# Kernel tuning notes

Measured on AMD Instinct MI355X. Metric: run time of the kernel, lower is better.

The kernel has to match this reference:

```python
import jax, jax.numpy as jnp
import numpy as np
from jax import lax

# sym8 analysis low-pass filter (pywt.Wavelet('sym8').dec_lo, matches MATLAB Lo_D)
FL = 16
DEC_LO = np.array([-0.0033824159510061256, -0.0005421323317911481, 0.03169508781149298,
                   0.007607487324917605, -0.1432942383508097, -0.061273359067658524,
                   0.4813596512583722, 0.7771857517005235, 0.3644418948353314,
                   -0.051945838107709037, -0.027219029917056003, 0.049137179673607506,
                   0.003808752013890615, -0.01495225833704823, -0.0003029205147213668,
                   0.0018899503327594609])
REC_LO = DEC_LO[::-1]
REC_HI = ((-1.0) ** np.arange(FL)) * DEC_LO  # qmf: rec_hi[k] = (-1)^k * rec_lo[FL-1-k]
DEC_HI = REC_HI[::-1]
# lax.conv does correlation, np.convolve flips -> store flipped filters
_DEC_K = jnp.asarray(np.stack([DEC_LO[::-1], DEC_HI[::-1]])[:, None, :], dtype=jnp.float32)  # (2,1,16)
_REC_K = jnp.asarray(np.stack([REC_LO[::-1], REC_HI[::-1]])[None, :, :], dtype=jnp.float32)  # (1,2,16)
DN = ('NCH', 'OIH', 'NCH')


def _dwt(x):
    # single-level pywt dwt, mode='symmetric': pad FL-1 each side, full conv, take odd indices
    B, C, S = x.shape
    xe = jnp.pad(x.reshape(B * C, 1, S), ((0, 0), (0, 0), (FL - 1, FL - 1)), mode='symmetric')[..., 1:]
    y = lax.conv_general_dilated(xe, _DEC_K, (2,), 'VALID', dimension_numbers=DN)
    L = y.shape[-1]  # floor((S + FL - 1)/2)
    y = y.reshape(B, C, 2, L)
    return y[:, :, 0], y[:, :, 1]


def _idwt(a, d):
    # single-level pywt idwt: upsample (len 2L-1), full conv, trim FL-2 each side
    B, C, L = a.shape
    c = jnp.stack([a, d], axis=2).reshape(B * C, 2, L)
    y = lax.conv_general_dilated(c, _REC_K, (1,), [(1, 1)], lhs_dilation=(2,), dimension_numbers=DN)
    return y.reshape(B, C, y.shape[-1])  # length 2L - FL + 2


def _wavedec(x, level):
    ds = []
    a = x
    for _ in range(level):
        a, d = _dwt(a)
        ds.append(d)
    return a, ds[::-1]  # coarsest first, matching pywt [cA_n, cD_n, ..., cD_1]


def _waverec(a, ds):
    for d in ds:
        if a.shape[-1] == d.shape[-1] + 1:  # static shapes -> Python if is jit-safe
            a = a[..., :-1]
        a = _idwt(a, d)
    return a


def _c1(x, w, b):
    # 1x1 conv: w (O,C), x (B,C,L)
    return jnp.einsum('oc,bcl->bol', w, x) + b[:, None]


def _inorm(x, eps=1e-5):
    m = jnp.mean(x, axis=-1, keepdims=True)
    v = jnp.mean((x - m) ** 2, axis=-1, keepdims=True)
    return (x - m) * lax.rsqrt(v + eps)


def _block(x, w_w, w_b, ca_w, ca_b, cd_w, cd_b, m1_w, m1_b, m2_w, m2_b):
    xn = _inorm(x)
    xs = lax.conv_general_dilated(xn, w_w, (1,), [(1, 1)], dimension_numbers=DN) + w_b[:, None]
    level = cd_w.shape[0]
    a, ds = _wavedec(xn, level)
    a = _c1(a, ca_w, ca_b)
    ds = [_c1(d, cd_w[i], cd_b[i]) for i, d in enumerate(ds)]
    xw = _waverec(a, ds)[..., : xs.shape[-1]]
    xo = x + jax.nn.gelu(xw + xs, approximate=False)
    xon = _inorm(xo)
    h = jax.nn.gelu(_c1(xon, m1_w, m1_b), approximate=False)
    return xo + _c1(h, m2_w, m2_b)


def _forward(x, lift_w, lift_b, blk_w_w, blk_w_b, blk_ca_w, blk_ca_b, blk_cd_w, blk_cd_b,
             blk_m1_w, blk_m1_b, blk_m2_w, blk_m2_b, p1_w, p1_b, p2_w, p2_b):
    B, S = x.shape
    grid = jnp.broadcast_to(jnp.linspace(-1.0, 1.0, S, dtype=x.dtype)[None, None, :], (B, 1, S))
    h = jnp.concatenate([x[:, None, :], grid], axis=1)  # (B, 2, S)
    h = _c1(h, lift_w, lift_b)
    for i in range(blk_w_w.shape[0]):
        h = _block(h, blk_w_w[i], blk_w_b[i], blk_ca_w[i], blk_ca_b[i], blk_cd_w[i],
                   blk_cd_b[i], blk_m1_w[i], blk_m1_b[i], blk_m2_w[i], blk_m2_b[i])
    h = jax.nn.gelu(_c1(h, p1_w, p1_b), approximate=False)
    return _c1(h, p2_w, p2_b)


def setup_inputs():
    key = jax.random.key(0)
    ks = jax.random.split(key, 17)
    B, S, C, NB, LV = 16, 8192, 64, 4, 4
    H = 2 * C  # mlp_expansion=2
    f = jnp.float32
    rn = lambda k, shape, s: jax.random.normal(k, shape, dtype=f) * s
    return {
        'x': jax.random.normal(ks[0], (B, S), dtype=f),
        'lift_w': rn(ks[1], (C, 2), 0.5), 'lift_b': rn(ks[2], (C,), 0.05),
        'blk_w_w': rn(ks[3], (NB, C, C, 3), 0.07), 'blk_w_b': rn(ks[4], (NB, C), 0.05),
        'blk_ca_w': rn(ks[5], (NB, C, C), 0.12), 'blk_ca_b': rn(ks[6], (NB, C), 0.05),
        'blk_cd_w': rn(ks[7], (NB, LV, C, C), 0.12), 'blk_cd_b': rn(ks[8], (NB, LV, C), 0.05),
        'blk_m1_w': rn(ks[9], (NB, H, C), 0.12), 'blk_m1_b': rn(ks[10], (NB, H), 0.05),
        'blk_m2_w': rn(ks[11], (NB, C, H), 0.08), 'blk_m2_b': rn(ks[12], (NB, C), 0.05),
        'p1_w': rn(ks[13], (C // 2, C), 0.12), 'p1_b': rn(ks[14], (C // 2,), 0.05),
        'p2_w': rn(ks[15], (C, C // 2), 0.17), 'p2_b': rn(ks[16], (C,), 0.05),
    }


def reference(x, lift_w, lift_b, blk_w_w, blk_w_b, blk_ca_w, blk_ca_b, blk_cd_w, blk_cd_b,
              blk_m1_w, blk_m1_b, blk_m2_w, blk_m2_b, p1_w, p1_b, p2_w, p2_b):
    return _forward(x, lift_w, lift_b, blk_w_w, blk_w_b, blk_ca_w, blk_ca_b, blk_cd_w,
                    blk_cd_b, blk_m1_w, blk_m1_b, blk_m2_w, blk_m2_b, p1_w, p1_b, p2_w, p2_b)
```

## Files before the change

### kernel.cpp

```cpp
#include <hip/hip_runtime.h>
#include <math.h>

#define S_LEN 8192
#define B_N   16
#define NBC   1024
#define L1v 4103
#define L2v 2059
#define L3v 1037
#define L4v 526
#define LB1 4104
#define LB2 2064
#define LB3 1040
#define LB4 528

#define OFF_CONV 0
#define OFF_M1   49152
#define OFF_M2   81920
#define OFF_CD   114688
#define OFF_CA   180224
#define OFF_P1   196608
#define OFF_P2   198656
#define WTOT     200704

typedef __attribute__((ext_vector_type(8))) short bf16x8;
typedef __attribute__((ext_vector_type(4))) float f32x4;

__constant__ float c_dlo[16] = {
    -0.0033824159510061256f, -0.0005421323317911481f,  0.03169508781149298f,
     0.007607487324917605f,  -0.1432942383508097f,    -0.061273359067658524f,
     0.4813596512583722f,     0.7771857517005235f,     0.3644418948353314f,
    -0.05194583810770904f,   -0.027219029917056003f,   0.049137179673607506f,
     0.003808752013890615f,  -0.01495225833704823f,   -0.0003029205147213668f,
     0.0018899503327594609f
};
__constant__ float c_dhi[16] = {
    -0.0018899503327594609f, -0.0003029205147213668f,  0.01495225833704823f,
     0.003808752013890615f,  -0.049137179673607506f,  -0.027219029917056003f,
     0.05194583810770904f,    0.3644418948353314f,    -0.7771857517005235f,
     0.4813596512583722f,     0.061273359067658524f,  -0.1432942383508097f,
    -0.007607487324917605f,   0.03169508781149298f,    0.0005421323317911481f,
    -0.0033824159510061256f
};

__device__ __forceinline__ float gelu1(float x) {
    return 0.5f * x * (1.0f + erff(x * 0.70710678118654752f));
}
__device__ __forceinline__ float4 load4g(const float* __restrict__ row, int l, int L) {
    float4 v;
    if (l >= 0 && l + 3 < L) {
        v = *(const float4*)(row + l);
    } else {
        v.x = (l     >= 0 && l     < L) ? row[l]     : 0.f;
        v.y = (l + 1 >= 0 && l + 1 < L) ? row[l + 1] : 0.f;
        v.z = (l + 2 >= 0 && l + 2 < L) ? row[l + 2] : 0.f;
        v.w = (l + 3 >= 0 && l + 3 < L) ? row[l + 3] : 0.f;
    }
    return v;
}
__device__ __forceinline__ ushort f2bf(float f) {
    uint u = __float_as_uint(f);
    u += 0x7fffu + ((u >> 16) & 1u);
    return (ushort)(u >> 16);
}
__device__ __forceinline__ uint pack2bf(float a, float b) {
    return (uint)f2bf(a) | ((uint)f2bf(b) << 16);
}
__device__ __forceinline__ float bfu(ushort u) {
    return __uint_as_float(((uint)u) << 16);
}

__global__ __launch_bounds__(256) void prep_kernel(const float* __restrict__ convW,
                                                   const float* __restrict__ m1,
                                                   const float* __restrict__ m2,
                                                   const float* __restrict__ cd,
                                                   const float* __restrict__ ca,
                                                   const float* __restrict__ p1,
                                                   const float* __restrict__ p2,
                                                   ushort* __restrict__ wbuf) {
    int idx = blockIdx.x * 256 + threadIdx.x;
    if (idx >= WTOT) return;
    float v;
    if (idx < OFF_M1) {
        int i = idx / 12288, r = idx % 12288;
        int o = r / 192, k = r % 192;
        int tap = k >> 6, c = k & 63;
        v = convW[i * 12288 + o * 192 + c * 3 + tap];
    } else if (idx < OFF_M2) v = m1[idx - OFF_M1];
    else if (idx < OFF_CD)   v = m2[idx - OFF_M2];
    else if (idx < OFF_CA)   v = cd[idx - OFF_CD];
    else if (idx < OFF_P1)   v = ca[idx - OFF_CA];
    else if (idx < OFF_P2)   v = p1[idx - OFF_P1];
    else                     v = p2[idx - OFF_P2];
    wbuf[idx] = f2bf(v);
}

__global__ __launch_bounds__(256) void lift_kernel(const float* __restrict__ x,
                                                   const float* __restrict__ w,
                                                   const float* __restrict__ bias,
                                                   float* __restrict__ out) {
    int idx = blockIdx.x * 256 + threadIdx.x;
    int s = idx & (S_LEN - 1);
    int r = idx >> 13;
    int o = r & 63;
    int b = r >> 6;
    float g = -1.0f + 2.0f * (float)s / (float)(S_LEN - 1);
    out[idx] = fmaf(w[o * 2 + 0], x[b * S_LEN + s], fmaf(w[o * 2 + 1], g, bias[o]));
}

__global__ __launch_bounds__(256) void stats_kernel(const float* __restrict__ in,
                                                    float2* __restrict__ stats) {
    const int base = blockIdx.x * S_LEN;
    const int tid = threadIdx.x;
    float s = 0.f, ss = 0.f;
#pragma unroll
    for (int i = 0; i < 8; ++i) {
        float4 v = *(const float4*)(in + base + (tid + i * 256) * 4);
        s += v.x + v.y + v.z + v.w;
        ss = fmaf(v.x, v.x, fmaf(v.y, v.y, fmaf(v.z, v.z, fmaf(v.w, v.w, ss))));
    }
    for (int off = 32; off > 0; off >>= 1) {
        s  += __shfl_down(s, off, 64);
        ss += __shfl_down(ss, off, 64);
    }
    __shared__ float sh[8];
    int lane = tid & 63, wv = tid >> 6;
    if (lane == 0) { sh[wv] = s; sh[4 + wv] = ss; }
    __syncthreads();
    if (tid == 0) {
        float tot  = sh[0] + sh[1] + sh[2] + sh[3];
        float tot2 = sh[4] + sh[5] + sh[6] + sh[7];
        float mean = tot * (1.0f / S_LEN);
        float var  = tot2 * (1.0f / S_LEN) - mean * mean;
        stats[blockIdx.x] = make_float2(mean, rsqrtf(var + 1e-5f));
    }
}

#define CWP 200
#define CXP 72

__global__ __launch_bounds__(256) void conv3_mfma_kernel(const float* __restrict__ in,
                                                         ushort* __restrict__ out,
                                                         const ushort* __restrict__ Wbf,
                                                         const float* __restrict__ bias,
                                                         const float2* __restrict__ stats) {
    __shared__ ushort sW[64 * CWP];
    __shared__ ushort sXt[144 * CXP];
    const int b = blockIdx.y;
    const int n0 = blockIdx.x * 128;
    const int tid = threadIdx.x;

    {
        const int o = tid >> 2, q = tid & 3;
        const uint4* src = (const uint4*)(Wbf + o * 192 + q * 48);
        uint4* dst = (uint4*)(sW + o * CWP + q * 48);
#pragma unroll
        for (int i = 0; i < 6; ++i) dst[i] = src[i];
    }
    {
        const int ch = tid >> 2, q = tid & 3;
        const int rowi = b * 64 + ch;
        const float2 st = stats[rowi];
        const float* row = in + (size_t)rowi * S_LEN;
#pragma unroll
        for (int i = 0; i < 9; ++i) {
            int p = q * 36 + i * 4;
            int l = n0 - 8 + p;
            float4 v;
            if (l >= 0 && l + 3 < S_LEN) {
                v = *(const float4*)(row + l);
                v.x = (v.x - st.x) * st.y; v.y = (v.y - st.x) * st.y;
                v.z = (v.z - st.x) * st.y; v.w = (v.w - st.x) * st.y;
            } else {
                v.x = (l     >= 0 && l     < S_LEN) ? (row[l]     - st.x) * st.y : 0.f;
                v.y = (l + 1 >= 0 && l + 1 < S_LEN) ? (row[l + 1] - st.x) * st.y : 0.f;
                v.z = (l + 2 >= 0 && l + 2 < S_LEN) ? (row[l + 2] - st.x) * st.y : 0.f;
                v.w = (l + 3 >= 0 && l + 3 < S_LEN) ? (row[l + 3] - st.x) * st.y : 0.f;
            }
            sXt[(p + 0) * CXP + ch] = f2bf(v.x);
            sXt[(p + 1) * CXP + ch] = f2bf(v.y);
            sXt[(p + 2) * CXP + ch] = f2bf(v.z);
            sXt[(p + 3) * CXP + ch] = f2bf(v.w);
        }
    }
    __syncthreads();

    const int w = tid >> 6, l = tid & 63, g = l >> 4, c = l & 15;
    f32x4 acc[2][4];
#pragma unroll
    for (int mt = 0; mt < 4; ++mt) {
        float4 bv = *(const float4*)(bias + 16 * mt + 4 * g);
#pragma unroll
        for (int t = 0; t < 2; ++t) {
            acc[t][mt][0] = bv.x; acc[t][mt][1] = bv.y;
            acc[t][mt][2] = bv.z; acc[t][mt][3] = bv.w;
        }
    }
#pragma unroll
    for (int kk = 0; kk < 6; ++kk) {
        const int tap = kk >> 1;
        bf16x8 af[4];
#pragma unroll
        for (int mt = 0; mt < 4; ++mt)
            af[mt] = *(bf16x8*)(sW + (16 * mt + c) * CWP + kk * 32 + 8 * g);
#pragma unroll
        for (int t = 0; t < 2; ++t) {
            const int nl = 32 * w + 16 * t + c;
            const int p = nl + tap + 7;
            bf16x8 xb = *(bf16x8*)(sXt + p * CXP + (kk & 1) * 32 + 8 * g);
#pragma unroll
            for (int mt = 0; mt < 4; ++mt)
                acc[t][mt] = __builtin_amdgcn_mfma_f32_16x16x32_bf16(af[mt], xb, acc[t][mt], 0, 0, 0);
        }
    }
#pragma unroll
    for (int t = 0; t < 2; ++t) {
        const int nl = 32 * w + 16 * t + c;
#pragma unroll
        for (int mt = 0; mt < 4; ++mt)
#pragma unroll
            for (int r = 0; r < 4; ++r) {
                int m = 16 * mt + 4 * g + r;
                out[((size_t)(b * 64 + m)) * S_LEN + n0 + nl] = f2bf(acc[t][mt][r]);
            }
    }
}

#define WMP 72
#define WXP 136

__global__ __launch_bounds__(256) void wmix_kernel(ushort* __restrict__ d1,
                                                   ushort* __restrict__ d2,
                                                   ushort* __restrict__ d3,
                                                   ushort* __restrict__ d4,
                                                   ushort* __restrict__ a4,
                                                   const ushort* __restrict__ cdbf,
                                                   const float* __restrict__ cd_b,
                                                   const ushort* __restrict__ cabf,
                                                   const float* __restrict__ ca_b) {
    __shared__ ushort sW[64 * WMP];
    __shared__ ushort sX[64 * WXP];
    const int b = blockIdx.y;
    const int t = blockIdx.x;
    ushort* buf; const ushort* W; const float* bias; int L, LP, l0;
    if (t < 33)      { buf = d1; W = cdbf + 3 * 4096; bias = cd_b + 3 * 64; L = L1v; LP = LB1; l0 = t * 128; }
    else if (t < 50) { buf = d2; W = cdbf + 2 * 4096; bias = cd_b + 2 * 64; L = L2v; LP = LB2; l0 = (t - 33) * 128; }
    else if (t < 59) { buf = d3; W = cdbf + 1 * 4096; bias = cd_b + 1 * 64; L = L3v; LP = LB3; l0 = (t - 50) * 128; }
    else if (t < 64) { buf = d4; W = cdbf;            bias = cd_b;          L = L4v; LP = LB4; l0 = (t - 59) * 128; }
    else             { buf = a4; W = cabf;            bias = ca_b;          L = L4v; LP = LB4; l0 = (t - 64) * 128; }
    const int tid = threadIdx.x;
    {
        int row = tid >> 2, q = tid & 3;
        const uint4* src = (const uint4*)(W + row * 64 + q * 16);
        uint4* dst = (uint4*)(sW + row * WMP + q * 16);
        dst[0] = src[0]; dst[1] = src[1];
    }
    {
        int ch = tid >> 2, part = tid & 3;
        const ushort* src = buf + ((size_t)(b * 64 + ch)) * LP;
#pragma unroll
        for (int i = 0; i < 4; ++i) {
            int l = l0 + part * 32 + 8 * i;
            ushort* dst = sX + ch * WXP + part * 32 + 8 * i;
            if (l + 8 <= L) {
                *(uint4*)dst = *(const uint4*)(src + l);
            } else {
#pragma unroll
                for (int j = 0; j < 8; ++j)
                    dst[j] = (l + j < L) ? src[l + j] : (ushort)0;
            }
        }
    }
    __syncthreads();
    const int w = tid >> 6, l = tid & 63, g = l >> 4, c = l & 15;
    f32x4 acc[2][4];
#pragma unroll
    for (int mt = 0; mt < 4; ++mt) {
        float4 bv = *(const float4*)(bias + 16 * mt + 4 * g);
#pragma unroll
        for (int tt = 0; tt < 2; ++tt) {
            acc[tt][mt][0] = bv.x; acc[tt][mt][1] = bv.y;
            acc[tt][mt][2] = bv.z; acc[tt][mt][3] = bv.w;
        }
    }
#pragma unroll
    for (int kk = 0; kk < 2; ++kk) {
        bf16x8 af[4];
#pragma unroll
        for (int mt = 0; mt < 4; ++mt)
            af[mt] = *(bf16x8*)(sW + (16 * mt + c) * WMP + kk * 32 + 8 * g);
#pragma unroll
        for (int tt = 0; tt < 2; ++tt) {
            const int nl = 32 * w + 16 * tt + c;
            bf16x8 xb;
#pragma unroll
            for (int j = 0; j < 8; ++j)
                xb[j] = (short)sX[(kk * 32 + 8 * g + j) * WXP + nl];
#pragma unroll
            for (int mt = 0; mt < 4; ++mt)
                acc[tt][mt] = __builtin_amdgcn_mfma_f32_16x16x32_bf16(af[mt], xb, acc[tt][mt], 0, 0, 0);
        }
    }
#pragma unroll
    for (int tt = 0; tt < 2; ++tt) {
        const int nl = 32 * w + 16 * tt + c;
        if (l0 + nl < L) {
#pragma unroll
            for (int mt = 0; mt < 4; ++mt)
#pragma unroll
                for (int r = 0; r < 4; ++r) {
                    int m = 16 * mt + 4 * g + r;
                    buf[((size_t)(b * 64 + m)) * LP + l0 + nl] = f2bf(acc[tt][mt][r]);
                }
        }
    }
}

#define W1P 72
#define W2P 136
#define XP  66
#define MP  136

__global__ __launch_bounds__(256) void mlp_kernel(float* __restrict__ A,
                                                  const float2* __restrict__ stats,
                                                  const ushort* __restrict__ W1bf,
                                                  const float* __restrict__ b1,
                                                  const ushort* __restrict__ W2bf,
                                                  const float* __restrict__ b2) {
    __shared__ ushort sW1[128 * W1P];
    __shared__ ushort sW2[64 * W2P];
    __shared__ ushort sX [64 * XP];
    __shared__ ushort sMid[64 * MP];
    const int b  = blockIdx.y;
    const int n0 = blockIdx.x * 64;
    const int tid = threadIdx.x;

    {
#pragma unroll
        for (int e = tid; e < 1024; e += 256) {
            int row = e >> 3, q = e & 7;
            *(uint4*)(sW1 + row * W1P + q * 8) = *(const uint4*)(W1bf + row * 64 + q * 8);
        }
    }
    {
#pragma unroll
        for (int e = tid; e < 1024; e += 256) {
            int row = e >> 4, q = e & 15;
            *(uint4*)(sW2 + row * W2P + q * 8) = *(const uint4*)(W2bf + row * 128 + q * 8);
        }
    }
    {
        int ch = tid >> 2, part = tid & 3;
        float2 st = stats[b * 64 + ch];
        const float* src = A + ((size_t)(b * 64 + ch)) * S_LEN + n0 + part * 16;
        uint* dst = (uint*)(sX + ch * XP + part * 16);
#pragma unroll
        for (int i = 0; i < 4; ++i) {
            float4 v = *(const float4*)(src + 4 * i);
            v.x = (v.x - st.x) * st.y; v.y = (v.y - st.x) * st.y;
            v.z = (v.z - st.x) * st.y; v.w = (v.w - st.x) * st.y;
            dst[2 * i]     = pack2bf(v.x, v.y);
            dst[2 * i + 1] = pack2bf(v.z, v.w);
        }
    }
    __syncthreads();

    const int w = tid >> 6;
    const int l = tid & 63;
    const int g = l >> 4;
    const int c = l & 15;
    const int nl = 16 * w + c;

    bf16x8 xb[2];
#pragma unroll
    for (int kk = 0; kk < 2; ++kk)
#pragma unroll
        for (int j = 0; j < 8; ++j)
            xb[kk][j] = (short)sX[(kk * 32 + 8 * g + j) * XP + nl];

    f32x4 acc1[8];
#pragma unroll
    for (int mt = 0; mt < 8; ++mt) {
        float4 bv = *(const float4*)(b1 + 16 * mt + 4 * g);
        acc1[mt][0] = bv.x; acc1[mt][1] = bv.y; acc1[mt][2] = bv.z; acc1[mt][3] = bv.w;
    }
#pragma unroll
    for (int kk = 0; kk < 2; ++kk) {
#pragma unroll
        for (int mt = 0; mt < 8; ++mt) {
            bf16x8 af = *(bf16x8*)(sW1 + (16 * mt + c) * W1P + kk * 32 + 8 * g);
            acc1[mt] = __builtin_amdgcn_mfma_f32_16x16x32_bf16(af, xb[kk], acc1[mt], 0, 0, 0);
        }
    }
#pragma unroll
    for (int mt = 0; mt < 8; ++mt) {
        uint* mp = (uint*)(sMid + nl * MP + 16 * mt + 4 * g);
        mp[0] = pack2bf(gelu1(acc1[mt][0]), gelu1(acc1[mt][1]));
        mp[1] = pack2bf(gelu1(acc1[mt][2]), gelu1(acc1[mt][3]));
    }

    bf16x8 mb[4];
#pragma unroll
    for (int kk = 0; kk < 4; ++kk)
        mb[kk] = *(bf16x8*)(sMid + nl * MP + kk * 32 + 8 * g);

    f32x4 acc2[4];
#pragma unroll
    for (int mt = 0; mt < 4; ++mt) {
        float4 bv = *(const float4*)(b2 + 16 * mt + 4 * g);
        acc2[mt][0] = bv.x; acc2[mt][1] = bv.y; acc2[mt][2] = bv.z; acc2[mt][3] = bv.w;
    }
#pragma unroll
    for (int kk = 0; kk < 4; ++kk) {
#pragma unroll
        for (int mt = 0; mt < 4; ++mt) {
            bf16x8 af = *(bf16x8*)(sW2 + (16 * mt + c) * W2P + kk * 32 + 8 * g);
            acc2[mt] = __builtin_amdgcn_mfma_f32_16x16x32_bf16(af, mb[kk], acc2[mt], 0, 0, 0);
        }
    }
#pragma unroll
    for (int mt = 0; mt < 4; ++mt) {
#pragma unroll
        for (int r = 0; r < 4; ++r) {
            int m = 16 * mt + 4 * g + r;
            float* p = A + ((size_t)(b * 64 + m)) * S_LEN + n0 + nl;
            *p = acc2[mt][r] + *p;
        }
    }
}

#define HXP 66
#define HMP 40

__global__ __launch_bounds__(256) void head_kernel(const float* __restrict__ A,
                                                   float* __restrict__ out,
                                                   const ushort* __restrict__ W1bf,
                                                   const float* __restrict__ b1,
                                                   const ushort* __restrict__ W2bf,
                                                   const float* __restrict__ b2) {
    __shared__ ushort sW1[32 * 72];
    __shared__ ushort sW2[64 * HMP];
    __shared__ ushort sX [64 * HXP];
    __shared__ ushort sMid[64 * HMP];
    const int b = blockIdx.y, n0 = blockIdx.x * 64, tid = threadIdx.x;
    {
        int row = tid >> 3, q = tid & 7;
        *(uint4*)(sW1 + row * 72 + q * 8) = *(const uint4*)(W1bf + row * 64 + q * 8);
    }
    {
        int row = tid >> 2, q = tid & 3;
        *(uint4*)(sW2 + row * HMP + q * 8) = *(const uint4*)(W2bf + row * 32 + q * 8);
    }
    {
        int ch = tid >> 2, part = tid & 3;
        const float* src = A + ((size_t)(b * 64 + ch)) * S_LEN + n0 + part * 16;
        uint* dst = (uint*)(sX + ch * HXP + part * 16);
#pragma unroll
        for (int i = 0; i < 4; ++i) {
            float4 v = *(const float4*)(src + 4 * i);
            dst[2 * i] = pack2bf(v.x, v.y); dst[2 * i + 1] = pack2bf(v.z, v.w);
        }
    }
    __syncthreads();
    const int w = tid >> 6, l = tid & 63, g = l >> 4, c = l & 15;
    const int nl = 16 * w + c;
    bf16x8 xb[2];
#pragma unroll
    for (int kk = 0; kk < 2; ++kk)
#pragma unroll
        for (int j = 0; j < 8; ++j)
            xb[kk][j] = (short)sX[(kk * 32 + 8 * g + j) * HXP + nl];
    f32x4 acc1[2];
#pragma unroll
    for (int mt = 0; mt < 2; ++mt) {
        float4 bv = *(const float4*)(b1 + 16 * mt + 4 * g);
        acc1[mt][0] = bv.x; acc1[mt][1] = bv.y; acc1[mt][2] = bv.z; acc1[mt][3] = bv.w;
    }
#pragma unroll
    for (int kk = 0; kk < 2; ++kk)
#pragma unroll
        for (int mt = 0; mt < 2; ++mt) {
            bf16x8 af = *(bf16x8*)(sW1 + (16 * mt + c) * 72 + kk * 32 + 8 * g);
            acc1[mt] = __builtin_amdgcn_mfma_f32_16x16x32_bf16(af, xb[kk], acc1[mt], 0, 0, 0);
        }
#pragma unroll
    for (int mt = 0; mt < 2; ++mt)
#pragma unroll
        for (int r = 0; r < 4; ++r)
            sMid[nl * HMP + 16 * mt + 4 * g + r] = f2bf(gelu1(acc1[mt][r]));
    bf16x8 mb = *(bf16x8*)(sMid + nl * HMP + 8 * g);
    f32x4 acc2[4];
#pragma unroll
    for (int mt = 0; mt < 4; ++mt) {
        float4 bv = *(const float4*)(b2 + 16 * mt + 4 * g);
        acc2[mt][0] = bv.x; acc2[mt][1] = bv.y; acc2[mt][2] = bv.z; acc2[mt][3] = bv.w;
    }
#pragma unroll
    for (int mt = 0; mt < 4; ++mt) {
        bf16x8 af = *(bf16x8*)(sW2 + (16 * mt + c) * HMP + 8 * g);
        acc2[mt] = __builtin_amdgcn_mfma_f32_16x16x32_bf16(af, mb, acc2[mt], 0, 0, 0);
    }
#pragma unroll
    for (int mt = 0; mt < 4; ++mt)
#pragma unroll
        for (int r = 0; r < 4; ++r) {
            int m = 16 * mt + 4 * g + r;
            out[((size_t)(b * 64 + m)) * S_LEN + n0 + nl] = acc2[mt][r];
        }
}

__device__ __forceinline__ void dwt8_core(const float* __restrict__ xb,
                                          float* __restrict__ lo, float* __restrict__ hi) {
#pragma unroll
    for (int j = 0; j < 8; ++j) {
        float l0 = 0.f, h0 = 0.f;
#pragma unroll
        for (int k = 0; k < 16; ++k) {
            float v = xb[2 * j + k + 2];
            l0 = fmaf(v, c_dlo[15 - k], l0);
            h0 = fmaf(v, c_dhi[15 - k], h0);
        }
        lo[j] = l0; hi[j] = h0;
    }
}

__device__ __forceinline__ void store_bf8(ushort* __restrict__ dst, int t0, int Lout,
                                          const float* __restrict__ v) {
    if (t0 + 8 <= Lout) {
        uint4 u;
        u.x = pack2bf(v[0], v[1]); u.y = pack2bf(v[2], v[3]);
        u.z = pack2bf(v[4], v[5]); u.w = pack2bf(v[6], v[7]);
        *(uint4*)(dst + t0) = u;
    } else {
#pragma unroll
        for (int j = 0; j < 8; ++j)
            if (t0 + j < Lout) dst[t0 + j] = f2bf(v[j]);
    }
}

__device__ __forceinline__ void dwt_lds_v2(const float* __restrict__ in, int Sin,
                                           float* __restrict__ aout,
                                           ushort* __restrict__ dout_g, int Lout, int tid) {
    const int NT = (Lout + 7) >> 3;
    for (int g = tid; g < NT; g += 256) {
        float xb[32];
        const int base = 16 * g - 16;
        if (base >= 0 && base + 32 <= Sin) {
#pragma unroll
            for (int q = 0; q < 8; ++q)
                *(float4*)(xb + 4 * q) = *(const float4*)(in + base + 4 * q);
        } else {
#pragma unroll
            for (int loc = 0; loc < 32; ++loc) {
                int i = base + loc;
                i = (i < 0) ? (-1 - i) : i;
                i = (i >= Sin) ? (2 * Sin - 1 - i) : i;
                xb[loc] = in[i];
            }
        }
        float lo[8], hi[8];
        dwt8_core(xb, lo, hi);
        const int t0 = 8 * g;
        if (t0 + 8 <= Lout) {
            *(float4*)(aout + t0)     = make_float4(lo[0], lo[1], lo[2], lo[3]);
            *(float4*)(aout + t0 + 4) = make_float4(lo[4], lo[5], lo[6], lo[7]);
        } else {
#pragma unroll
            for (int j = 0; j < 8; ++j) if (t0 + j < Lout) aout[t0 + j] = lo[j];
        }
        store_bf8(dout_g, t0, Lout, hi);
    }
}

__global__ __launch_bounds__(256) void dwt_full_kernel(const float* __restrict__ A,
                                                       const float2* __restrict__ stats,
                                                       ushort* __restrict__ d1,
                                                       ushort* __restrict__ d2,
                                                       ushort* __restrict__ d3,
                                                       ushort* __restrict__ d4,
                                                       ushort* __restrict__ a4) {
    __shared__ float bufA[4104];
    __shared__ float bufB[2064];
    const int row = blockIdx.x;
    const int tid = threadIdx.x;
    const float2 st = stats[row];
    const float* x = A + (size_t)row * S_LEN;
    ushort* d1r = d1 + (size_t)row * LB1;

    for (int g = tid; g < 513; g += 256) {
        const int base = 16 * g - 16;
        float xb[32];
        if (base >= 0 && base + 32 <= S_LEN) {
#pragma unroll
            for (int q = 0; q < 8; ++q) {
                float4 v = *(const float4*)(x + base + 4 * q);
                v.x = (v.x - st.x) * st.y; v.y = (v.y - st.x) * st.y;
                v.z = (v.z - st.x) * st.y; v.w = (v.w - st.x) * st.y;
                *(float4*)(xb + 4 * q) = v;
            }
        } else {
#pragma unroll
            for (int loc = 0; loc < 32; ++loc) {
                int i = base + loc;
                i = (i < 0) ? (-1 - i) : i;
                i = (i >= S_LEN) ? (2 * S_LEN - 1 - i) : i;
                xb[loc] = (x[i] - st.x) * st.y;
            }
        }
        float lo[8], hi[8];
        dwt8_core(xb, lo, hi);
        const int t0 = 8 * g;
#pragma unroll
        for (int j = 0; j < 8; ++j)
            if (t0 + j < L1v) bufA[t0 + j] = lo[j];
        store_bf8(d1r, t0, L1v, hi);
    }
    __syncthreads();
    dwt_lds_v2(bufA, L1v, bufB, d2 + (size_t)row * LB2, L2v, tid);
    __syncthreads();
    dwt_lds_v2(bufB, L2v, bufA, d3 + (size_t)row * LB3, L3v, tid);
    __syncthreads();
    dwt_lds_v2(bufA, L3v, bufB, d4 + (size_t)row * LB4, L4v, tid);
    __syncthreads();
    ushort* a4r = a4 + (size_t)row * LB4;
    for (int g = tid; g < 66; g += 256) {
        const int t0 = 8 * g;
        float v[8];
#pragma unroll
        for (int j = 0; j < 8; ++j)
            v[j] = (t0 + j < L4v) ? bufB[t0 + j] : 0.f;
        store_bf8(a4r, t0, 528, v);
    }
}

__device__ __forceinline__ void idwt8_regs(const float* __restrict__ a,
                                           const float* __restrict__ d,
                                           int g, int Lc, float* __restrict__ y) {
    float av[12], dv[12];
    const int m0 = 4 * g;
    if (m0 + 12 <= Lc) {
#pragma unroll
        for (int q = 0; q < 3; ++q) {
            *(float4*)(av + 4 * q) = *(const float4*)(a + m0 + 4 * q);
            *(float4*)(dv + 4 * q) = *(const float4*)(d + m0 + 4 * q);
        }
    } else {
#pragma unroll
        for (int jj = 0; jj < 12; ++jj) {
            int m = m0 + jj;
            bool ok = (m < Lc);
            av[jj] = ok ? a[m] : 0.f;
            dv[jj] = ok ? d[m] : 0.f;
        }
    }
#pragma unroll
    for (int e = 0; e < 4; ++e) {
        float ye = 0.f, yo = 0.f;
#pragma unroll
        for (int j = 0; j < 8; ++j) {
            ye = fmaf(av[e + j], c_dlo[2 * j + 1], ye);
            ye = fmaf(dv[e + j], c_dlo[14 - 2 * j], ye);
            yo = fmaf(av[e + j], c_dlo[2 * j], yo);
            yo = fmaf(dv[e + j], -c_dlo[15 - 2 * j], yo);
        }
        y[2 * e] = ye;
        y[2 * e + 1] = yo;
    }
}

__device__ __forceinline__ void idwt_lds_v2(const float* __restrict__ a,
                                            const float* __restrict__ d,
                                            int Lc, int Lout, float* __restrict__ out, int tid) {
    const int NT = (Lout + 7) >> 3;
    for (int g = tid; g < NT; g += 256) {
        float y[8];
        idwt8_regs(a, d, g, Lc, y);
        const int t0 = 8 * g;
        if (t0 + 8 <= Lout) {
            *(float4*)(out + t0)     = make_float4(y[0], y[1], y[2], y[3]);
            *(float4*)(out + t0 + 4) = make_float4(y[4], y[5], y[6], y[7]);
        } else {
#pragma unroll
            for (int j = 0; j < 8; ++j) if (t0 + j < Lout) out[t0 + j] = y[j];
        }
    }
}

__device__ __forceinline__ void gload_lds_bf(const ushort* __restrict__ src, int Lv,
                                             float* __restrict__ dst, int tid) {
    const int NG = (Lv + 7) >> 3;
    for (int g = tid; g < NG; g += 256) {
        uint4 u = *(const uint4*)(src + 8 * g);
        float v[8];
        v[0] = bfu((ushort)u.x); v[1] = bfu((ushort)(u.x >> 16));
        v[2] = bfu((ushort)u.y); v[3] = bfu((ushort)(u.y >> 16));
        v[4] = bfu((ushort)u.z); v[5] = bfu((ushort)(u.z >> 16));
        v[6] = bfu((ushort)u.w); v[7] = bfu((ushort)(u.w >> 16));
        const int t0 = 8 * g;
#pragma unroll
        for (int j = 0; j < 8; ++j)
            dst[t0 + j] = (t0 + j < Lv) ? v[j] : 0.f;
    }
}

__global__ __launch_bounds__(256) void idwt_full_kernel(const ushort* __restrict__ a4,
                                                        const ushort* __restrict__ d4,
                                                        const ushort* __restrict__ d3,
                                                        const ushort* __restrict__ d2,
                                                        const ushort* __restrict__ d1,
                                                        float* __restrict__ h,
                                                        const ushort* __restrict__ xs,
                                                        float2* __restrict__ statsOut) {
    __shared__ float bufY[4104];
    __shared__ float bufA[4104];
    __shared__ float bufD[4104];
    const int row = blockIdx.x;
    const int tid = threadIdx.x;

    gload_lds_bf(a4 + (size_t)row * LB4, L4v, bufA, tid);
    gload_lds_bf(d4 + (size_t)row * LB4, L4v, bufD, tid);
    __syncthreads();
    idwt_lds_v2(bufA, bufD, L4v, 1038, bufY, tid);
    __syncthreads();
    gload_lds_bf(d3 + (size_t)row * LB3, L3v, bufD, tid);
    __syncthreads();
    idwt_lds_v2(bufY, bufD, L3v, 2060, bufA, tid);
    __syncthreads();
    gload_lds_bf(d2 + (size_t)row * LB2, L2v, bufD, tid);
    __syncthreads();
    idwt_lds_v2(bufA, bufD, L2v, 4104, bufY, tid);
    __syncthreads();
    gload_lds_bf(d1 + (size_t)row * LB1, L1v, bufD, tid);
    __syncthreads();

    float* hrow = h + (size_t)row * S_LEN;
    const ushort* srow = xs + (size_t)row * S_LEN;
    float s = 0.f, ss = 0.f;
#pragma unroll
    for (int it = 0; it < 4; ++it) {
        const int g = it * 256 + tid;
        float y[8];
        idwt8_regs(bufY, bufD, g, L1v, y);
        const int t0 = 8 * g;
#pragma unroll
        for (int q = 0; q < 2; ++q) {
            uint2 sp = *(const uint2*)(srow + t0 + 4 * q);
            float4 hv = *(const float4*)(hrow + t0 + 4 * q);
            hv.x += gelu1(y[4 * q + 0] + bfu((ushort)sp.x));
            hv.y += gelu1(y[4 * q + 1] + bfu((ushort)(sp.x >> 16)));
            hv.z += gelu1(y[4 * q + 2] + bfu((ushort)sp.y));
            hv.w += gelu1(y[4 * q + 3] + bfu((ushort)(sp.y >> 16)));
            *(float4*)(hrow + t0 + 4 * q) = hv;
            s += hv.x + hv.y + hv.z + hv.w;
            ss = fmaf(hv.x, hv.x, fmaf(hv.y, hv.y, fmaf(hv.z, hv.z, fmaf(hv.w, hv.w, ss))));
        }
    }
    for (int off = 32; off > 0; off >>= 1) {
        s  += __shfl_down(s, off, 64);
        ss += __shfl_down(ss, off, 64);
    }
    __syncthreads();
    int lane = tid & 63, wv = tid >> 6;
    if (lane == 0) { bufA[wv] = s; bufA[4 + wv] = ss; }
    __syncthreads();
    if (tid == 0) {
        float tot  = bufA[0] + bufA[1] + bufA[2] + bufA[3];
        float tot2 = bufA[4] + bufA[5] + bufA[6] + bufA[7];
        float mean = tot * (1.0f / S_LEN);
        float var  = tot2 * (1.0f / S_LEN) - mean * mean;
        statsOut[row] = make_float2(mean, rsqrtf(var + 1e-5f));
    }
}

extern "C" void kernel_launch(void* const* d_in, const int* in_sizes, int n_in,
                              void* d_out, int out_size, void* d_ws, size_t ws_size,
                              hipStream_t stream) {
    const float* x       = (const float*)d_in[0];
    const float* lift_w  = (const float*)d_in[1];
    const float* lift_b  = (const float*)d_in[2];
    const float* blk_w_w = (const float*)d_in[3];
    const float* blk_w_b = (const float*)d_in[4];
    const float* blk_ca_w= (const float*)d_in[5];
    const float* blk_ca_b= (const float*)d_in[6];
    const float* blk_cd_w= (const float*)d_in[7];
    const float* blk_cd_b= (const float*)d_in[8];
    const float* blk_m1_w= (const float*)d_in[9];
    const float* blk_m1_b= (const float*)d_in[10];
    const float* blk_m2_w= (const float*)d_in[11];
    const float* blk_m2_b= (const float*)d_in[12];
    const float* p1_w    = (const float*)d_in[13];
    const float* p1_b    = (const float*)d_in[14];
    const float* p2_w    = (const float*)d_in[15];
    const float* p2_b    = (const float*)d_in[16];

    float* ws = (float*)d_ws;
    const size_t T32 = (size_t)NBC * S_LEN;
    float* A  = ws;
    ushort* Cc = (ushort*)(ws + T32);
    ushort* d1 = Cc + T32;
    ushort* d2 = d1 + (size_t)NBC * LB1;
    ushort* d3 = d2 + (size_t)NBC * LB2;
    ushort* d4 = d3 + (size_t)NBC * LB3;
    ushort* a4 = d4 + (size_t)NBC * LB4;
    float2* statsBuf = (float2*)(a4 + (size_t)NBC * LB4 + 8);
    ushort* wbuf = (ushort*)(statsBuf + NBC);

    dim3 blk(256);

    prep_kernel<<<(WTOT + 255) / 256, blk, 0, stream>>>(blk_w_w, blk_m1_w, blk_m2_w,
                                                        blk_cd_w, blk_ca_w, p1_w, p2_w, wbuf);
    lift_kernel<<<(NBC * S_LEN) / 256, blk, 0, stream>>>(x, lift_w, lift_b, A);

    for (int i = 0; i < 4; ++i) {
        const float* w_b  = blk_w_b  + (size_t)i * 64;
        const float* ca_b = blk_ca_b + (size_t)i * 64;
        const float* cd_b = blk_cd_b + (size_t)i * 4 * 64;
        const float* m1_b = blk_m1_b + (size_t)i * 128;
        const float* m2_b = blk_m2_b + (size_t)i * 64;
        const ushort* convbf = wbuf + OFF_CONV + (size_t)i * 12288;
        const ushort* m1bf   = wbuf + OFF_M1   + (size_t)i * 8192;
        const ushort* m2bf   = wbuf + OFF_M2   + (size_t)i * 8192;
        const ushort* cdbf   = wbuf + OFF_CD   + (size_t)i * 16384;
        const ushort* cabf   = wbuf + OFF_CA   + (size_t)i * 4096;

        stats_kernel<<<NBC, blk, 0, stream>>>(A, statsBuf);
        conv3_mfma_kernel<<<dim3(S_LEN / 128, B_N), blk, 0, stream>>>(A, Cc, convbf, w_b, statsBuf);
        dwt_full_kernel<<<NBC, blk, 0, stream>>>(A, statsBuf, d1, d2, d3, d4, a4);

        wmix_kernel<<<dim3(69, B_N), blk, 0, stream>>>(d1, d2, d3, d4, a4,
                                                       cdbf, cd_b, cabf, ca_b);

        idwt_full_kernel<<<NBC, blk, 0, stream>>>(a4, d4, d3, d2, d1, A, Cc, statsBuf);
        mlp_kernel<<<dim3(S_LEN / 64, B_N), blk, 0, stream>>>(A, statsBuf, m1bf, m1_b, m2bf, m2_b);
    }

    head_kernel<<<dim3(S_LEN / 64, B_N), blk, 0, stream>>>(A, (float*)d_out,
                                                           wbuf + OFF_P1, p1_b,
                                                           wbuf + OFF_P2, p2_b);
}
```

Before: 682.0 us.

## Fuse row statistics into lift and MLP kernels via atomics, widen DWT blocks

```diff
diff --git a/kernel.cpp b/kernel.cpp
--- a/kernel.cpp
+++ b/kernel.cpp
@@ -45,18 +45,6 @@
 __device__ __forceinline__ float gelu1(float x) {
     return 0.5f * x * (1.0f + erff(x * 0.70710678118654752f));
 }
-__device__ __forceinline__ float4 load4g(const float* __restrict__ row, int l, int L) {
-    float4 v;
-    if (l >= 0 && l + 3 < L) {
-        v = *(const float4*)(row + l);
-    } else {
-        v.x = (l     >= 0 && l     < L) ? row[l]     : 0.f;
-        v.y = (l + 1 >= 0 && l + 1 < L) ? row[l + 1] : 0.f;
-        v.z = (l + 2 >= 0 && l + 2 < L) ? row[l + 2] : 0.f;
-        v.w = (l + 3 >= 0 && l + 3 < L) ? row[l + 3] : 0.f;
-    }
-    return v;
-}
 __device__ __forceinline__ ushort f2bf(float f) {
     uint u = __float_as_uint(f);
     u += 0x7fffu + ((u >> 16) & 1u);
@@ -67,6 +55,11 @@
 }
 __device__ __forceinline__ float bfu(ushort u) {
     return __uint_as_float(((uint)u) << 16);
+}
+__device__ __forceinline__ float2 raw2stat(float2 r) {
+    float mean = r.x * (1.0f / S_LEN);
+    float var  = r.y * (1.0f / S_LEN) - mean * mean;
+    return make_float2(mean, rsqrtf(var + 1e-5f));
 }
 
 __global__ __launch_bounds__(256) void prep_kernel(const float* __restrict__ convW,
@@ -76,8 +69,10 @@
                                                    const float* __restrict__ ca,
                                                    const float* __restrict__ p1,
                                                    const float* __restrict__ p2,
-                                                   ushort* __restrict__ wbuf) {
+                                                   ushort* __restrict__ wbuf,
+                                                   float* __restrict__ statsRawF) {
     int idx = blockIdx.x * 256 + threadIdx.x;
+    if (idx < 2048) statsRawF[idx] = 0.f;
     if (idx >= WTOT) return;
     float v;
     if (idx < OFF_M1) {
@@ -97,41 +92,33 @@
 __global__ __launch_bounds__(256) void lift_kernel(const float* __restrict__ x,
                                                    const float* __restrict__ w,
                                                    const float* __restrict__ bias,
-                                                   float* __restrict__ out) {
-    int idx = blockIdx.x * 256 + threadIdx.x;
-    int s = idx & (S_LEN - 1);
-    int r = idx >> 13;
-    int o = r & 63;
-    int b = r >> 6;
-    float g = -1.0f + 2.0f * (float)s / (float)(S_LEN - 1);
-    out[idx] = fmaf(w[o * 2 + 0], x[b * S_LEN + s], fmaf(w[o * 2 + 1], g, bias[o]));
-}
-
-__global__ __launch_bounds__(256) void stats_kernel(const float* __restrict__ in,
-                                                    float2* __restrict__ stats) {
-    const int base = blockIdx.x * S_LEN;
-    const int tid = threadIdx.x;
-    float s = 0.f, ss = 0.f;
-#pragma unroll
-    for (int i = 0; i < 8; ++i) {
-        float4 v = *(const float4*)(in + base + (tid + i * 256) * 4);
-        s += v.x + v.y + v.z + v.w;
-        ss = fmaf(v.x, v.x, fmaf(v.y, v.y, fmaf(v.z, v.z, fmaf(v.w, v.w, ss))));
-    }
+                                                   float* __restrict__ out,
+                                                   float* __restrict__ statsRawF) {
+    const size_t base = (size_t)blockIdx.x * 1024 + threadIdx.x * 4;
+    const int row = (int)(base >> 13);
+    const int o = row & 63, b = row >> 6;
+    const int s0 = (int)(base & (S_LEN - 1));
+    const float w0 = w[o * 2], w1 = w[o * 2 + 1], bv = bias[o];
+    float4 xv = *(const float4*)(x + (size_t)b * S_LEN + s0);
+    float4 v;
+    v.x = fmaf(w0, xv.x, fmaf(w1, -1.f + 2.f * (float)(s0    ) / (float)(S_LEN - 1), bv));
+    v.y = fmaf(w0, xv.y, fmaf(w1, -1.f + 2.f * (float)(s0 + 1) / (float)(S_LEN - 1), bv));
+    v.z = fmaf(w0, xv.z, fmaf(w1, -1.f + 2.f * (float)(s0 + 2) / (float)(S_LEN - 1), bv));
+    v.w = fmaf(w0, xv.w, fmaf(w1, -1.f + 2.f * (float)(s0 + 3) / (float)(S_LEN - 1), bv));
+    *(float4*)(out + base) = v;
+    float s  = v.x + v.y + v.z + v.w;
+    float ss = fmaf(v.x, v.x, fmaf(v.y, v.y, fmaf(v.z, v.z, v.w * v.w)));
     for (int off = 32; off > 0; off >>= 1) {
         s  += __shfl_down(s, off, 64);
         ss += __shfl_down(ss, off, 64);
     }
     __shared__ float sh[8];
-    int lane = tid & 63, wv = tid >> 6;
+    int lane = threadIdx.x & 63, wv = threadIdx.x >> 6;
     if (lane == 0) { sh[wv] = s; sh[4 + wv] = ss; }
     __syncthreads();
-    if (tid == 0) {
-        float tot  = sh[0] + sh[1] + sh[2] + sh[3];
-        float tot2 = sh[4] + sh[5] + sh[6] + sh[7];
-        float mean = tot * (1.0f / S_LEN);
-        float var  = tot2 * (1.0f / S_LEN) - mean * mean;
-        stats[blockIdx.x] = make_float2(mean, rsqrtf(var + 1e-5f));
+    if (threadIdx.x == 0) {
+        atomicAdd(&statsRawF[row * 2 + 0], sh[0] + sh[1] + sh[2] + sh[3]);
+        atomicAdd(&statsRawF[row * 2 + 1], sh[4] + sh[5] + sh[6] + sh[7]);
     }
 }
 
@@ -142,7 +129,7 @@
                                                          ushort* __restrict__ out,
                                                          const ushort* __restrict__ Wbf,
                                                          const float* __restrict__ bias,
-                                                         const float2* __restrict__ stats) {
+                                                         const float2* __restrict__ statsRaw) {
     __shared__ ushort sW[64 * CWP];
     __shared__ ushort sXt[144 * CXP];
     const int b = blockIdx.y;
@@ -159,7 +146,7 @@
     {
         const int ch = tid >> 2, q = tid & 3;
         const int rowi = b * 64 + ch;
-        const float2 st = stats[rowi];
+        const float2 st = raw2stat(statsRaw[rowi]);
         const float* row = in + (size_t)rowi * S_LEN;
 #pragma unroll
         for (int i = 0; i < 9; ++i) {
@@ -236,18 +223,22 @@
                                                    const ushort* __restrict__ cdbf,
                                                    const float* __restrict__ cd_b,
                                                    const ushort* __restrict__ cabf,
-                                                   const float* __restrict__ ca_b) {
+                                                   const float* __restrict__ ca_b,
+                                                   float* __restrict__ statsRawF) {
     __shared__ ushort sW[64 * WMP];
     __shared__ ushort sX[64 * WXP];
     const int b = blockIdx.y;
     const int t = blockIdx.x;
+    const int tid = threadIdx.x;
+    if (t == 68 && b == 0) {
+        for (int e = tid; e < 2048; e += 256) statsRawF[e] = 0.f;
+    }
     ushort* buf; const ushort* W; const float* bias; int L, LP, l0;
     if (t < 33)      { buf = d1; W = cdbf + 3 * 4096; bias = cd_b + 3 * 64; L = L1v; LP = LB1; l0 = t * 128; }
     else if (t < 50) { buf = d2; W = cdbf + 2 * 4096; bias = cd_b + 2 * 64; L = L2v; LP = LB2; l0 = (t - 33) * 128; }
     else if (t < 59) { buf = d3; W = cdbf + 1 * 4096; bias = cd_b + 1 * 64; L = L3v; LP = LB3; l0 = (t - 50) * 128; }
     else if (t < 64) { buf = d4; W = cdbf;            bias = cd_b;          L = L4v; LP = LB4; l0 = (t - 59) * 128; }
     else             { buf = a4; W = cabf;            bias = ca_b;          L = L4v; LP = LB4; l0 = (t - 64) * 128; }
-    const int tid = threadIdx.x;
     {
         int row = tid >> 2, q = tid & 3;
         const uint4* src = (const uint4*)(W + row * 64 + q * 16);
@@ -321,7 +312,9 @@
 #define MP  136
 
 __global__ __launch_bounds__(256) void mlp_kernel(float* __restrict__ A,
-                                                  const float2* __restrict__ stats,
+                                                  const float2* __restrict__ statsB,
+                                                  float* __restrict__ statsRawF,
+                                                  int doStats,
                                                   const ushort* __restrict__ W1bf,
                                                   const float* __restrict__ b1,
                                                   const ushort* __restrict__ W2bf,
@@ -350,7 +343,7 @@
     }
     {
         int ch = tid >> 2, part = tid & 3;
-        float2 st = stats[b * 64 + ch];
+        float2 st = statsB[b * 64 + ch];
         const float* src = A + ((size_t)(b * 64 + ch)) * S_LEN + n0 + part * 16;
         uint* dst = (uint*)(sX + ch * XP + part * 16);
 #pragma unroll
@@ -403,6 +396,8 @@
     for (int kk = 0; kk < 4; ++kk)
         mb[kk] = *(bf16x8*)(sMid + nl * MP + kk * 32 + 8 * g);
 
+    if (doStats) __syncthreads();
+
     f32x4 acc2[4];
 #pragma unroll
     for (int mt = 0; mt < 4; ++mt) {
@@ -417,13 +412,33 @@
             acc2[mt] = __builtin_amdgcn_mfma_f32_16x16x32_bf16(af, mb[kk], acc2[mt], 0, 0, 0);
         }
     }
+    float* sMidF = (float*)sMid;
 #pragma unroll
     for (int mt = 0; mt < 4; ++mt) {
 #pragma unroll
         for (int r = 0; r < 4; ++r) {
             int m = 16 * mt + 4 * g + r;
             float* p = A + ((size_t)(b * 64 + m)) * S_LEN + n0 + nl;
-            *p = acc2[mt][r] + *p;
+            float v = acc2[mt][r] + *p;
+            *p = v;
+            if (doStats) sMidF[m * 64 + nl] = v;
+        }
+    }
+    if (doStats) {
+        __syncthreads();
+        const int row = tid >> 2, part = tid & 3;
+        float s = 0.f, ss = 0.f;
+#pragma unroll
+        for (int j = 0; j < 16; ++j) {
+            float v = sMidF[row * 64 + part * 16 + j];
+            s += v;
+            ss = fmaf(v, v, ss);
+        }
+        s  += __shfl_xor(s, 1, 64);  s  += __shfl_xor(s, 2, 64);
+        ss += __shfl_xor(ss, 1, 64); ss += __shfl_xor(ss, 2, 64);
+        if (part == 0) {
+            atomicAdd(&statsRawF[(b * 64 + row) * 2 + 0], s);
+            atomicAdd(&statsRawF[(b * 64 + row) * 2 + 1], ss);
         }
     }
 }
@@ -539,9 +554,10 @@
 
 __device__ __forceinline__ void dwt_lds_v2(const float* __restrict__ in, int Sin,
                                            float* __restrict__ aout,
-                                           ushort* __restrict__ dout_g, int Lout, int tid) {
+                                           ushort* __restrict__ dout_g, int Lout,
+                                           int tid, int nthr) {
     const int NT = (Lout + 7) >> 3;
-    for (int g = tid; g < NT; g += 256) {
+    for (int g = tid; g < NT; g += nthr) {
         float xb[32];
         const int base = 16 * g - 16;
         if (base >= 0 && base + 32 <= Sin) {
@@ -571,8 +587,8 @@
     }
 }
 
-__global__ __launch_bounds__(256) void dwt_full_kernel(const float* __restrict__ A,
-                                                       const float2* __restrict__ stats,
+__global__ __launch_bounds__(512) void dwt_full_kernel(const float* __restrict__ A,
+                                                       const float2* __restrict__ statsRaw,
                                                        ushort* __restrict__ d1,
                                                        ushort* __restrict__ d2,
                                                        ushort* __restrict__ d3,
@@ -582,11 +598,11 @@
     __shared__ float bufB[2064];
     const int row = blockIdx.x;
     const int tid = threadIdx.x;
-    const float2 st = stats[row];
+    const float2 st = raw2stat(statsRaw[row]);
     const float* x = A + (size_t)row * S_LEN;
     ushort* d1r = d1 + (size_t)row * LB1;
 
-    for (int g = tid; g < 513; g += 256) {
+    for (int g = tid; g < 513; g += 512) {
         const int base = 16 * g - 16;
         float xb[32];
         if (base >= 0 && base + 32 <= S_LEN) {
@@ -615,14 +631,14 @@
         store_bf8(d1r, t0, L1v, hi);
     }
     __syncthreads();
-    dwt_lds_v2(bufA, L1v, bufB, d2 + (size_t)row * LB2, L2v, tid);
-    __syncthreads();
-    dwt_lds_v2(bufB, L2v, bufA, d3 + (size_t)row * LB3, L3v, tid);
-    __syncthreads();
-    dwt_lds_v2(bufA, L3v, bufB, d4 + (size_t)row * LB4, L4v, tid);
+    dwt_lds_v2(bufA, L1v, bufB, d2 + (size_t)row * LB2, L2v, tid, 512);
+    __syncthreads();
+    dwt_lds_v2(bufB, L2v, bufA, d3 + (size_t)row * LB3, L3v, tid, 512);
+    __syncthreads();
+    dwt_lds_v2(bufA, L3v, bufB, d4 + (size_t)row * LB4, L4v, tid, 512);
     __syncthreads();
     ushort* a4r = a4 + (size_t)row * LB4;
-    for (int g = tid; g < 66; g += 256) {
+    for (int g = tid; g < 66; g += 512) {
         const int t0 = 8 * g;
         float v[8];
 #pragma unroll
@@ -669,9 +685,10 @@
 
 __device__ __forceinline__ void idwt_lds_v2(const float* __restrict__ a,
                                             const float* __restrict__ d,
-                                            int Lc, int Lout, float* __restrict__ out, int tid) {
+                                            int Lc, int Lout, float* __restrict__ out,
+                                            int tid, int nthr) {
     const int NT = (Lout + 7) >> 3;
-    for (int g = tid; g < NT; g += 256) {
+    for (int g = tid; g < NT; g += nthr) {
         float y[8];
         idwt8_regs(a, d, g, Lc, y);
         const int t0 = 8 * g;
@@ -686,9 +703,9 @@
 }
 
 __device__ __forceinline__ void gload_lds_bf(const ushort* __restrict__ src, int Lv,
-                                             float* __restrict__ dst, int tid) {
+                                             float* __restrict__ dst, int tid, int nthr) {
     const int NG = (Lv + 7) >> 3;
-    for (int g = tid; g < NG; g += 256) {
+    for (int g = tid; g < NG; g += nthr) {
         uint4 u = *(const uint4*)(src + 8 * g);
         float v[8];
         v[0] = bfu((ushort)u.x); v[1] = bfu((ushort)(u.x >> 16));
@@ -702,42 +719,42 @@
     }
 }
 
-__global__ __launch_bounds__(256) void idwt_full_kernel(const ushort* __restrict__ a4,
+__global__ __launch_bounds__(512) void idwt_full_kernel(const ushort* __restrict__ a4,
                                                         const ushort* __restrict__ d4,
                                                         const ushort* __restrict__ d3,
                                                         const ushort* __restrict__ d2,
                                                         const ushort* __restrict__ d1,
                                                         float* __restrict__ h,
                                                         const ushort* __restrict__ xs,
-                                                        float2* __restrict__ statsOut) {
+                                                        float2* __restrict__ statsB) {
     __shared__ float bufY[4104];
     __shared__ float bufA[4104];
     __shared__ float bufD[4104];
     const int row = blockIdx.x;
     const int tid = threadIdx.x;
 
-    gload_lds_bf(a4 + (size_t)row * LB4, L4v, bufA, tid);
-    gload_lds_bf(d4 + (size_t)row * LB4, L4v, bufD, tid);
-    __syncthreads();
-    idwt_lds_v2(bufA, bufD, L4v, 1038, bufY, tid);
-    __syncthreads();
-    gload_lds_bf(d3 + (size_t)row * LB3, L3v, bufD, tid);
-    __syncthreads();
-    idwt_lds_v2(bufY, bufD, L3v, 2060, bufA, tid);
-    __syncthreads();
-    gload_lds_bf(d2 + (size_t)row * LB2, L2v, bufD, tid);
-    __syncthreads();
-    idwt_lds_v2(bufA, bufD, L2v, 4104, bufY, tid);
-    __syncthreads();
-    gload_lds_bf(d1 + (size_t)row * LB1, L1v, bufD, tid);
+    gload_lds_bf(a4 + (size_t)row * LB4, L4v, bufA, tid, 512);
+    gload_lds_bf(d4 + (size_t)row * LB4, L4v, bufD, tid, 512);
+    __syncthreads();
+    idwt_lds_v2(bufA, bufD, L4v, 1038, bufY, tid, 512);
+    __syncthreads();
+    gload_lds_bf(d3 + (size_t)row * LB3, L3v, bufD, tid, 512);
+    __syncthreads();
+    idwt_lds_v2(bufY, bufD, L3v, 2060, bufA, tid, 512);
+    __syncthreads();
+    gload_lds_bf(d2 + (size_t)row * LB2, L2v, bufD, tid, 512);
+    __syncthreads();
+    idwt_lds_v2(bufA, bufD, L2v, 4104, bufY, tid, 512);
+    __syncthreads();
+    gload_lds_bf(d1 + (size_t)row * LB1, L1v, bufD, tid, 512);
     __syncthreads();
 
     float* hrow = h + (size_t)row * S_LEN;
     const ushort* srow = xs + (size_t)row * S_LEN;
     float s = 0.f, ss = 0.f;
 #pragma unroll
-    for (int it = 0; it < 4; ++it) {
-        const int g = it * 256 + tid;
+    for (int it = 0; it < 2; ++it) {
+        const int g = it * 512 + tid;
         float y[8];
         idwt8_regs(bufY, bufD, g, L1v, y);
         const int t0 = 8 * g;
@@ -760,14 +777,15 @@
     }
     __syncthreads();
     int lane = tid & 63, wv = tid >> 6;
-    if (lane == 0) { bufA[wv] = s; bufA[4 + wv] = ss; }
+    if (lane == 0) { bufA[wv] = s; bufA[8 + wv] = ss; }
     __syncthreads();
     if (tid == 0) {
-        float tot  = bufA[0] + bufA[1] + bufA[2] + bufA[3];
-        float tot2 = bufA[4] + bufA[5] + bufA[6] + bufA[7];
+        float tot = 0.f, tot2 = 0.f;
+#pragma unroll
+        for (int i = 0; i < 8; ++i) { tot += bufA[i]; tot2 += bufA[8 + i]; }
         float mean = tot * (1.0f / S_LEN);
         float var  = tot2 * (1.0f / S_LEN) - mean * mean;
-        statsOut[row] = make_float2(mean, rsqrtf(var + 1e-5f));
+        statsB[row] = make_float2(mean, rsqrtf(var + 1e-5f));
     }
 }
 
@@ -801,14 +819,17 @@
     ushort* d3 = d2 + (size_t)NBC * LB2;
     ushort* d4 = d3 + (size_t)NBC * LB3;
     ushort* a4 = d4 + (size_t)NBC * LB4;
-    float2* statsBuf = (float2*)(a4 + (size_t)NBC * LB4 + 8);
-    ushort* wbuf = (ushort*)(statsBuf + NBC);
+    float2* statsRaw = (float2*)(a4 + (size_t)NBC * LB4 + 8);
+    float2* statsB   = statsRaw + NBC;
+    ushort* wbuf = (ushort*)(statsB + NBC);
 
     dim3 blk(256);
+    dim3 blk512(512);
 
     prep_kernel<<<(WTOT + 255) / 256, blk, 0, stream>>>(blk_w_w, blk_m1_w, blk_m2_w,
-                                                        blk_cd_w, blk_ca_w, p1_w, p2_w, wbuf);
-    lift_kernel<<<(NBC * S_LEN) / 256, blk, 0, stream>>>(x, lift_w, lift_b, A);
+                                                        blk_cd_w, blk_ca_w, p1_w, p2_w,
+                                                        wbuf, (float*)statsRaw);
+    lift_kernel<<<(NBC * S_LEN) / 1024, blk, 0, stream>>>(x, lift_w, lift_b, A, (float*)statsRaw);
 
     for (int i = 0; i < 4; ++i) {
         const float* w_b  = blk_w_b  + (size_t)i * 64;
@@ -822,15 +843,16 @@
         const ushort* cdbf   = wbuf + OFF_CD   + (size_t)i * 16384;
         const ushort* cabf   = wbuf + OFF_CA   + (size_t)i * 4096;
 
-        stats_kernel<<<NBC, blk, 0, stream>>>(A, statsBuf);
-        conv3_mfma_kernel<<<dim3(S_LEN / 128, B_N), blk, 0, stream>>>(A, Cc, convbf, w_b, statsBuf);
-        dwt_full_kernel<<<NBC, blk, 0, stream>>>(A, statsBuf, d1, d2, d3, d4, a4);
+        conv3_mfma_kernel<<<dim3(S_LEN / 128, B_N), blk, 0, stream>>>(A, Cc, convbf, w_b, statsRaw);
+        dwt_full_kernel<<<NBC, blk512, 0, stream>>>(A, statsRaw, d1, d2, d3, d4, a4);
 
         wmix_kernel<<<dim3(69, B_N), blk, 0, stream>>>(d1, d2, d3, d4, a4,
-                                                       cdbf, cd_b, cabf, ca_b);
-
-        idwt_full_kernel<<<NBC, blk, 0, stream>>>(a4, d4, d3, d2, d1, A, Cc, statsBuf);
-        mlp_kernel<<<dim3(S_LEN / 64, B_N), blk, 0, stream>>>(A, statsBuf, m1bf, m1_b, m2bf, m2_b);
+                                                       cdbf, cd_b, cabf, ca_b, (float*)statsRaw);
+
+        idwt_full_kernel<<<NBC, blk512, 0, stream>>>(a4, d4, d3, d2, d1, A, Cc, statsB);
+        mlp_kernel<<<dim3(S_LEN / 64, B_N), blk, 0, stream>>>(A, statsB, (float*)statsRaw,
+                                                              (i < 3) ? 1 : 0,
+                                                              m1bf, m1_b, m2bf, m2_b);
     }
 
     head_kernel<<<dim3(S_LEN / 64, B_N), blk, 0, stream>>>(A, (float*)d_out,
```

Measured after the change: 715.3 us. +4.9%, slower.
